# Kernel tuning notes

Hardware: AMD Instinct MI355X
Metric: run time of the kernel (lower is better)

## Reference

```python
import jax, jax.numpy as jnp
import numpy as np

N = 50000      # nodes
E = 1600000    # edges (before self loops)
G = 64         # graphs in batch
DIN = 128
HID = 64
H = 4
NEG_SLOPE = 0.2
BN_EPS = 1e-5


def setup_inputs() -> dict:
    key = jax.random.key(0)
    ks = jax.random.split(key, 32)
    p = lambda i, shape: 0.1 * jax.random.normal(ks[i], shape, dtype=jnp.float32)
    inp = {
        "x": jax.random.normal(ks[0], (N, DIN), dtype=jnp.float32),
        "edge_index": jax.random.randint(ks[1], (2, E), 0, N),
        "batch": jnp.sort(jax.random.randint(ks[2], (N,), 0, G)),
        # GAT layer 1: DIN -> HID x H heads (concat)
        "W1": p(3, (DIN, H * HID)),
        "att_src1": p(4, (H, HID)),
        "att_dst1": p(5, (H, HID)),
        "bias1": p(6, (H * HID,)),
        "bn1_g": jnp.ones((H * HID,), jnp.float32),
        "bn1_b": jnp.zeros((H * HID,), jnp.float32),
        "bn1_m": p(7, (H * HID,)),
        "bn1_v": jnp.ones((H * HID,), jnp.float32),
        # GAT layer 2: H*HID -> HID, 1 head
        "W2": p(8, (H * HID, HID)),
        "att_src2": p(9, (1, HID)),
        "att_dst2": p(10, (1, HID)),
        "bias2": p(11, (HID,)),
        "bn2_g": jnp.ones((HID,), jnp.float32),
        "bn2_b": jnp.zeros((HID,), jnp.float32),
        "bn2_m": p(12, (HID,)),
        "bn2_v": jnp.ones((HID,), jnp.float32),
        # classifier
        "Wc1": p(13, (HID, HID)),
        "bc1": p(14, (HID,)),
        "Wc2": p(15, (HID, 2)),
        "bc2": p(16, (2,)),
    }
    return inp


def _gat_layer(x, src, dst, W, a_src, a_dst, bias, heads, n):
    # x: [n, F_in]; src/dst: [E'] (self loops included)
    c = W.shape[1] // heads
    xw = (x @ W).reshape(n, heads, c)                       # [n, H, C]
    alpha_s = jnp.sum(xw * a_src, axis=-1)                  # [n, H]
    alpha_d = jnp.sum(xw * a_dst, axis=-1)                  # [n, H]
    e = alpha_s[src] + alpha_d[dst]                         # [E', H]
    e = jnp.where(e >= 0, e, NEG_SLOPE * e)                 # leaky relu
    # softmax over incoming edges of each dst node
    m = jax.ops.segment_max(e, dst, num_segments=n)         # [n, H]
    ex = jnp.exp(e - m[dst])
    denom = jax.ops.segment_sum(ex, dst, num_segments=n)    # [n, H]
    w = ex / (denom[dst] + 1e-16)                           # [E', H]
    out = jax.ops.segment_sum(xw[src] * w[:, :, None], dst, num_segments=n)
    return out.reshape(n, heads * c) + bias


def _bn_eval(x, g, b, m, v):
    return (x - m) * (g / jnp.sqrt(v + BN_EPS)) + b


def reference(x, edge_index, batch,
              W1, att_src1, att_dst1, bias1, bn1_g, bn1_b, bn1_m, bn1_v,
              W2, att_src2, att_dst2, bias2, bn2_g, bn2_b, bn2_m, bn2_v,
              Wc1, bc1, Wc2, bc2):
    n = x.shape[0]
    loops = jnp.arange(n, dtype=edge_index.dtype)
    src = jnp.concatenate([edge_index[0], loops])  # PyG GATConv adds self loops
    dst = jnp.concatenate([edge_index[1], loops])

    h = _gat_layer(x, src, dst, W1, att_src1, att_dst1, bias1, H, n)
    h = jax.nn.relu(_bn_eval(h, bn1_g, bn1_b, bn1_m, bn1_v))
    # residual skipped: dims (256) vs x (128) mismatch -> not added, as in torch code

    h2 = _gat_layer(h, src, dst, W2, att_src2, att_dst2, bias2, 1, n)
    h2 = jax.nn.relu(_bn_eval(h2, bn2_g, bn2_b, bn2_m, bn2_v))
    # residual skipped: 64 vs 256 mismatch

    # global mean pool over each graph
    sums = jax.ops.segment_sum(h2, batch, num_segments=G)
    cnt = jax.ops.segment_sum(jnp.ones((n,), h2.dtype), batch, num_segments=G)
    graph_repr = sums / jnp.maximum(cnt, 1.0)[:, None]      # [G, HID]

    hc = jax.nn.relu(graph_repr @ Wc1 + bc1)
    logits = hc @ Wc2 + bc2
    return jax.nn.log_softmax(logits, axis=1)
```

## Files before the change

### kernel.cpp

```cpp
#include <hip/hip_runtime.h>

#define NEG_SLOPE 0.2f
#define CAP1 224
#define CAP2 224
#define CAPB 5120
#define EPB  16384

typedef short bf16x8 __attribute__((ext_vector_type(8)));
typedef float f32x4  __attribute__((ext_vector_type(4)));
typedef float f32x2  __attribute__((ext_vector_type(2)));

static __device__ __forceinline__ float u16f(unsigned short u){
  union { unsigned int i; float f; } v; v.i = ((unsigned int)u) << 16; return v.f;
}
static __device__ __forceinline__ unsigned short f2u16(float f){
  union { float f; unsigned int i; } v; v.f = f;
  unsigned int r = (v.i + 0x7FFFu + ((v.i >> 16) & 1u)) >> 16;
  return (unsigned short)r;
}
static __device__ __forceinline__ unsigned char f2fp8(float f){
  int w = __builtin_amdgcn_cvt_pk_fp8_f32(f, f, 0, false);
  return (unsigned char)(w & 0xFF);
}
static __device__ __forceinline__ float fp82f(unsigned char b){
  f32x2 d = __builtin_amdgcn_cvt_pk_f32_fp8((int)b, false);
  return d[0];
}
static __device__ __forceinline__ float wsum(float v){
  #pragma unroll
  for (int o = 32; o > 0; o >>= 1) v += __shfl_xor(v, o, 64);
  return v;
}
static __device__ __forceinline__ float qsum(float v){
  #pragma unroll
  for (int o = 1; o < 16; o <<= 1) v += __shfl_xor(v, o, 64);
  return v;
}
static __device__ __forceinline__ float lrelu(float e){
  return e >= 0.f ? e : NEG_SLOPE * e;
}

__global__ __launch_bounds__(256) void k_zero(int* __restrict__ p, int nwords){
  int i = blockIdx.x * 256 + threadIdx.x;
  if (i < nwords) p[i] = 0;
}

__global__ __launch_bounds__(256) void k_cvt(const float* __restrict__ x,
                                             unsigned short* __restrict__ xb, int n4){
  int i = blockIdx.x * 256 + threadIdx.x;
  if (i >= n4) return;
  float4 f = ((const float4*)x)[i];
  ushort4 u;
  u.x = f2u16(f.x); u.y = f2u16(f.y); u.z = f2u16(f.z); u.w = f2u16(f.w);
  ((ushort4*)xb)[i] = u;
}

__global__ __launch_bounds__(256) void k_pack1(const float* __restrict__ W1,
                                               unsigned short* __restrict__ B1p){
  int idx = blockIdx.x * 256 + threadIdx.x;
  if (idx >= 4*16*64*8) return;
  int j = idx & 7, lane = (idx >> 3) & 63, nt = (idx >> 9) & 15, kc = idx >> 13;
  int k = kc*32 + (lane >> 4)*8 + j;
  int n = nt*16 + (lane & 15);
  B1p[idx] = f2u16(W1[k*256 + n]);
}

__global__ __launch_bounds__(256) void k_pack2(const float* __restrict__ W2,
                                               unsigned short* __restrict__ B2p){
  int idx = blockIdx.x * 256 + threadIdx.x;
  if (idx >= 8*4*64*8) return;
  int j = idx & 7, lane = (idx >> 3) & 63, nt = (idx >> 9) & 3, kc = idx >> 11;
  int k = kc*32 + (lane >> 4)*8 + j;
  int n = nt*16 + (lane & 15);
  B2p[idx] = f2u16(W2[k*64 + n]);
}

__global__ __launch_bounds__(256) void k_gemm1m(
    const unsigned short* __restrict__ xb, const bf16x8* __restrict__ B1p,
    const float* __restrict__ asrc, const float* __restrict__ adst,
    unsigned char* __restrict__ xw1, float* __restrict__ oas, float* __restrict__ oad,
    int N)
{
  __shared__ unsigned short xs[64][136];
  int t = threadIdx.x;
  int m0 = blockIdx.x * 64;
  #pragma unroll
  for (int i = 0; i < 4; ++i){
    int flat = t + i*256;
    int r = flat >> 4, c8 = flat & 15;
    uint4 v = make_uint4(0,0,0,0);
    if (m0 + r < N) v = *(const uint4*)(xb + (size_t)(m0 + r)*128 + c8*8);
    *(uint4*)&xs[r][c8*8] = v;
  }
  __syncthreads();
  int w = t >> 6, l = t & 63;
  int quad = l >> 4, ml = l & 15;

  f32x4 acc[16];
  #pragma unroll
  for (int i = 0; i < 16; ++i){ acc[i][0]=0.f; acc[i][1]=0.f; acc[i][2]=0.f; acc[i][3]=0.f; }

  #pragma unroll
  for (int kc = 0; kc < 4; ++kc){
    bf16x8 a = *(const bf16x8*)&xs[w*16 + ml][kc*32 + quad*8];
    #pragma unroll
    for (int nt = 0; nt < 16; ++nt){
      bf16x8 b = B1p[(kc*16 + nt)*64 + l];
      acc[nt] = __builtin_amdgcn_mfma_f32_16x16x32_bf16(a, b, acc[nt], 0, 0, 0);
    }
  }

  float as_h[4][4], ad_h[4][4];
  #pragma unroll
  for (int h = 0; h < 4; ++h)
    #pragma unroll
    for (int r = 0; r < 4; ++r){ as_h[h][r] = 0.f; ad_h[h][r] = 0.f; }
  #pragma unroll
  for (int nt = 0; nt < 16; ++nt){
    float vs = asrc[nt*16 + ml], vd = adst[nt*16 + ml];
    int h = nt >> 2;
    #pragma unroll
    for (int r = 0; r < 4; ++r){
      as_h[h][r] += acc[nt][r] * vs;
      ad_h[h][r] += acc[nt][r] * vd;
    }
  }
  #pragma unroll
  for (int h = 0; h < 4; ++h)
    #pragma unroll
    for (int r = 0; r < 4; ++r){ as_h[h][r] = qsum(as_h[h][r]); ad_h[h][r] = qsum(ad_h[h][r]); }

  int baserow = m0 + w*16 + quad*4;
  if (ml == 0){
    #pragma unroll
    for (int r = 0; r < 4; ++r){
      int node = baserow + r;
      if (node < N){
        *(float4*)(oas + (size_t)node*4) = make_float4(as_h[0][r], as_h[1][r], as_h[2][r], as_h[3][r]);
        *(float4*)(oad + (size_t)node*4) = make_float4(ad_h[0][r], ad_h[1][r], ad_h[2][r], ad_h[3][r]);
      }
    }
  }
  #pragma unroll
  for (int r = 0; r < 4; ++r){
    int node = baserow + r;
    if (node >= N) continue;
    #pragma unroll
    for (int nt = 0; nt < 16; ++nt)
      xw1[(size_t)node*256 + nt*16 + ml] = f2fp8(acc[nt][r]);
  }
}

__global__ __launch_bounds__(256) void k_gemm2m(
    const unsigned short* __restrict__ h1, const bf16x8* __restrict__ B2p,
    const float* __restrict__ asrc, const float* __restrict__ adst,
    unsigned char* __restrict__ xw2, float* __restrict__ oas, float* __restrict__ oad,
    int N)
{
  __shared__ unsigned short ys[64][264];
  int t = threadIdx.x;
  int m0 = blockIdx.x * 64;
  #pragma unroll
  for (int i = 0; i < 8; ++i){
    int flat = t + i*256;
    int r = flat >> 5, c8 = flat & 31;
    uint4 v = make_uint4(0,0,0,0);
    if (m0 + r < N) v = *(const uint4*)(h1 + (size_t)(m0 + r)*256 + c8*8);
    *(uint4*)&ys[r][c8*8] = v;
  }
  __syncthreads();
  int w = t >> 6, l = t & 63;
  int quad = l >> 4, ml = l & 15;

  f32x4 acc[4];
  #pragma unroll
  for (int i = 0; i < 4; ++i){ acc[i][0]=0.f; acc[i][1]=0.f; acc[i][2]=0.f; acc[i][3]=0.f; }

  #pragma unroll
  for (int kc = 0; kc < 8; ++kc){
    bf16x8 a = *(const bf16x8*)&ys[w*16 + ml][kc*32 + quad*8];
    #pragma unroll
    for (int nt = 0; nt < 4; ++nt){
      bf16x8 b = B2p[(kc*4 + nt)*64 + l];
      acc[nt] = __builtin_amdgcn_mfma_f32_16x16x32_bf16(a, b, acc[nt], 0, 0, 0);
    }
  }

  float as_p[4] = {0,0,0,0}, ad_p[4] = {0,0,0,0};
  #pragma unroll
  for (int nt = 0; nt < 4; ++nt){
    float vs = asrc[nt*16 + ml], vd = adst[nt*16 + ml];
    #pragma unroll
    for (int r = 0; r < 4; ++r){
      as_p[r] += acc[nt][r] * vs;
      ad_p[r] += acc[nt][r] * vd;
    }
  }
  #pragma unroll
  for (int r = 0; r < 4; ++r){ as_p[r] = qsum(as_p[r]); ad_p[r] = qsum(ad_p[r]); }

  int baserow = m0 + w*16 + quad*4;
  if (ml == 0){
    #pragma unroll
    for (int r = 0; r < 4; ++r){
      int node = baserow + r;
      if (node < N){ oas[node] = as_p[r]; oad[node] = ad_p[r]; }
    }
  }
  #pragma unroll
  for (int r = 0; r < 4; ++r){
    int node = baserow + r;
    if (node >= N) continue;
    #pragma unroll
    for (int nt = 0; nt < 4; ++nt)
      xw2[(size_t)node*64 + nt*16 + ml] = f2fp8(acc[nt][r]);
  }
}

__global__ __launch_bounds__(256) void k_hist(const int* __restrict__ ei,
                                              int* __restrict__ count, int E, int ET){
  int i = blockIdx.x * 256 + threadIdx.x;
  if (i >= ET) return;
  int d = (i < E) ? ei[E + i] : (i - E);
  atomicAdd(&count[d], 1);
}

__global__ __launch_bounds__(256) void k_scan1(const int* __restrict__ count,
                                               int* __restrict__ ro, int* __restrict__ bsum, int N){
  __shared__ int sd[256];
  int t = threadIdx.x, b = blockIdx.x, i = b*256 + t;
  int v = (i < N) ? count[i] : 0;
  sd[t] = v; __syncthreads();
  for (int o = 1; o < 256; o <<= 1){
    int x = (t >= o) ? sd[t - o] : 0;
    __syncthreads();
    sd[t] += x;
    __syncthreads();
  }
  if (i < N) ro[i] = sd[t] - v;
  if (t == 255) bsum[b] = sd[255];
}

__global__ __launch_bounds__(256) void k_scan2(int* __restrict__ bsum, int nb){
  __shared__ int sd[256];
  int t = threadIdx.x;
  int v = (t < nb) ? bsum[t] : 0;
  sd[t] = v; __syncthreads();
  for (int o = 1; o < 256; o <<= 1){
    int x = (t >= o) ? sd[t - o] : 0;
    __syncthreads();
    sd[t] += x;
    __syncthreads();
  }
  if (t < nb) bsum[t] = sd[t] - v;
}

__global__ __launch_bounds__(256) void k_scan3(int* __restrict__ ro,
                                               const int* __restrict__ bsum, int N, int ET){
  int b = blockIdx.x, t = threadIdx.x, i = b*256 + t;
  if (i < N) ro[i] += bsum[b];
  if (b == 0 && t == 0) ro[N] = ET;
}

__global__ __launch_bounds__(1024) void k_binscat(const int* __restrict__ ei,
                                                  const int* __restrict__ ro,
                                                  int* __restrict__ bincur,
                                                  int* __restrict__ binbuf,
                                                  int* __restrict__ cursor,
                                                  int* __restrict__ csr,
                                                  int E, int ET, int NB){
  __shared__ int lhist[512];
  __shared__ int lbase[512];
  __shared__ int lcur[512];
  int t = threadIdx.x;
  int base = blockIdx.x * EPB;
  for (int i = t; i < 512; i += 1024){ lhist[i] = 0; lcur[i] = 0; }
  __syncthreads();

  int myb[16], mypay[16];
  #pragma unroll
  for (int k = 0; k < 16; ++k){
    int i = base + t + k*1024;
    int b = -1, pay = 0;
    if (i < ET){
      int s, d;
      if (i < E){ s = ei[i]; d = ei[E + i]; }
      else      { s = i - E; d = i - E; }
      b = d >> 7;
      pay = ((d & 127) << 16) | s;
      atomicAdd(&lhist[b], 1);
    }
    myb[k] = b; mypay[k] = pay;
  }
  __syncthreads();

  for (int i = t; i < NB; i += 1024){
    int h = lhist[i];
    if (h > 0) lbase[i] = atomicAdd(&bincur[i * 16], h);
  }
  __syncthreads();

  #pragma unroll
  for (int k = 0; k < 16; ++k){
    int b = myb[k];
    if (b < 0) continue;
    int pos = lbase[b] + atomicAdd(&lcur[b], 1);
    if (pos < CAPB){
      binbuf[(size_t)b * CAPB + pos] = mypay[k];
    } else {
      int d = (b << 7) | (mypay[k] >> 16);
      int s = mypay[k] & 0xFFFF;
      int posr = atomicAdd(&cursor[d], 1);
      csr[ro[d + 1] - 1 - posr] = s;
    }
  }
}

__global__ __launch_bounds__(256) void k_binsort(const int* __restrict__ bincur,
                                                 const int* __restrict__ binbuf,
                                                 const int* __restrict__ ro,
                                                 int* __restrict__ csr, int N){
  __shared__ int rolocal[129];
  __shared__ int lcnt[128];
  __shared__ int stage[CAPB];
  int b = blockIdx.x, t = threadIdx.x;
  int base = b << 7;
  int wn = N - base; if (wn > 128) wn = 128;
  if (wn <= 0) return;
  for (int i = t; i <= wn; i += 256) rolocal[i] = ro[base + i];
  for (int i = t; i < wn; i += 256) lcnt[i] = 0;
  __syncthreads();
  int rostart = rolocal[0];
  int seglen = rolocal[wn] - rostart;
  int total = bincur[b * 16];
  int cnt = total < CAPB ? total : CAPB;
  bool ovf = (seglen > CAPB) || (total > CAPB);
  const int* buf = binbuf + (size_t)b * CAPB;

  if (!ovf){
    for (int i = t; i < cnt; i += 256){
      int u = buf[i];
      int s = u & 0xFFFF, ld = u >> 16;
      int r = atomicAdd(&lcnt[ld], 1);
      stage[rolocal[ld] - rostart + r] = s;
    }
    __syncthreads();
    for (int i = t; i < seglen; i += 256) csr[rostart + i] = stage[i];
  } else {
    for (int i = t; i < cnt; i += 256){
      int u = buf[i];
      int s = u & 0xFFFF, ld = u >> 16;
      int r = atomicAdd(&lcnt[ld], 1);
      csr[rolocal[ld] + r] = s;
    }
  }
}

__global__ __launch_bounds__(256) void k_edge1(
    const int* __restrict__ ro, const int* __restrict__ cs,
    const unsigned char* __restrict__ xw1,
    const float* __restrict__ pas, const float* __restrict__ pad,
    const float* __restrict__ bias1,
    const float* __restrict__ g1, const float* __restrict__ b1,
    const float* __restrict__ m1, const float* __restrict__ v1,
    unsigned short* __restrict__ h1, int N)
{
  __shared__ float wt[4][CAP1][5];
  int t = threadIdx.x, w = t >> 6, lane = t & 63;
  int n = blockIdx.x * 4 + w;
  if (n >= N) return;
  int beg = ro[n], end = ro[n + 1], deg = end - beg;
  const float4 adv = *(const float4*)(pad + (size_t)n * 4);
  const bool fits = (deg <= CAP1);

  float s0 = 0.f, s1 = 0.f, s2 = 0.f, s3 = 0.f;
  for (int j = lane; j < deg; j += 64){
    int s = cs[beg + j];
    float4 a = *(const float4*)(pas + (size_t)s * 4);
    float e0 = __expf(lrelu(a.x + adv.x));
    float e1 = __expf(lrelu(a.y + adv.y));
    float e2 = __expf(lrelu(a.z + adv.z));
    float e3 = __expf(lrelu(a.w + adv.w));
    if (fits){
      wt[w][j][0] = e0; wt[w][j][1] = e1;
      wt[w][j][2] = e2; wt[w][j][3] = e3;
      wt[w][j][4] = __int_as_float(s << 8);
    }
    s0 += e0; s1 += e1; s2 += e2; s3 += e3;
  }
  s0 = wsum(s0); s1 = wsum(s1); s2 = wsum(s2); s3 = wsum(s3);

  int head = lane >> 4;
  float invh = 1.f / ((head == 0 ? s0 : head == 1 ? s1 : head == 2 ? s2 : s3) + 1e-16f);
  float aa   = head == 0 ? adv.x : head == 1 ? adv.y : head == 2 ? adv.z : adv.w;

  float a0 = 0.f, a1 = 0.f, a2 = 0.f, a3 = 0.f;
  if (fits){
    for (int j = 0; j < deg; ++j){
      float wv = wt[w][j][head] * invh;
      int off = __float_as_int(wt[w][j][4]);
      int u = *(const int*)(xw1 + off + lane * 4);
      f32x2 lo = __builtin_amdgcn_cvt_pk_f32_fp8(u, false);
      f32x2 hi = __builtin_amdgcn_cvt_pk_f32_fp8(u, true);
      a0 += wv * lo[0]; a1 += wv * lo[1];
      a2 += wv * hi[0]; a3 += wv * hi[1];
    }
  } else {
    for (int j = 0; j < deg; ++j){
      int s = cs[beg + j];
      float wv = __expf(lrelu(pas[(size_t)s * 4 + head] + aa)) * invh;
      int u = *(const int*)(xw1 + (size_t)s * 256 + lane * 4);
      f32x2 lo = __builtin_amdgcn_cvt_pk_f32_fp8(u, false);
      f32x2 hi = __builtin_amdgcn_cvt_pk_f32_fp8(u, true);
      a0 += wv * lo[0]; a1 += wv * lo[1];
      a2 += wv * hi[0]; a3 += wv * hi[1];
    }
  }

  float accv[4] = {a0, a1, a2, a3};
  ushort4 outv;
  unsigned short* po = (unsigned short*)&outv;
  int j0 = lane * 4;
  #pragma unroll
  for (int i = 0; i < 4; ++i){
    int j = j0 + i;
    float o  = accv[i] + bias1[j];
    float sc = g1[j] * rsqrtf(v1[j] + 1e-5f);
    float res = (o - m1[j]) * sc + b1[j];
    po[i] = f2u16(fmaxf(res, 0.f));
  }
  *(ushort4*)(h1 + (size_t)n * 256 + j0) = outv;
}

__global__ __launch_bounds__(256) void k_edge2(
    const int* __restrict__ ro, const int* __restrict__ cs,
    const unsigned char* __restrict__ xw2,
    const float* __restrict__ pas, const float* __restrict__ pad,
    const float* __restrict__ bias2,
    const float* __restrict__ g2, const float* __restrict__ b2,
    const float* __restrict__ m2, const float* __restrict__ v2,
    float* __restrict__ h2, int N)
{
  __shared__ float wt[4][CAP2][2];
  int t = threadIdx.x, w = t >> 6, lane = t & 63;
  int n = blockIdx.x * 4 + w;
  if (n >= N) return;
  int beg = ro[n], end = ro[n + 1], deg = end - beg;
  float adv = pad[n];
  const bool fits = (deg <= CAP2);

  float dh = 0.f;
  for (int j = lane; j < deg; j += 64){
    int s = cs[beg + j];
    float e = __expf(lrelu(pas[s] + adv));
    if (fits){
      wt[w][j][0] = e;
      wt[w][j][1] = __int_as_float(s << 6);
    }
    dh += e;
  }
  dh = wsum(dh);
  float inv = 1.f / (dh + 1e-16f);

  float acc = 0.f;
  if (fits){
    for (int j = 0; j < deg; ++j){
      float wv = wt[w][j][0] * inv;
      int off = __float_as_int(wt[w][j][1]);
      acc += wv * fp82f(xw2[off + lane]);
    }
  } else {
    for (int j = 0; j < deg; ++j){
      int s = cs[beg + j];
      float wv = __expf(lrelu(pas[s] + adv)) * inv;
      acc += wv * fp82f(xw2[(size_t)s * 64 + lane]);
    }
  }

  float o  = acc + bias2[lane];
  float sc = g2[lane] * rsqrtf(v2[lane] + 1e-5f);
  h2[(size_t)n * 64 + lane] = fmaxf((o - m2[lane]) * sc + b2[lane], 0.f);
}

__global__ __launch_bounds__(256) void k_pool(
    const float* __restrict__ h2, const int* __restrict__ batch,
    float* __restrict__ pool, int N)
{
  int g = blockIdx.x;
  int t = threadIdx.x, c = t & 63, w = t >> 6;
  int lo = 0, hi = N;
  while (lo < hi){ int mid = (lo + hi) >> 1; if (batch[mid] < g) lo = mid + 1; else hi = mid; }
  int lo2 = lo, hi2 = N;
  while (lo2 < hi2){ int mid = (lo2 + hi2) >> 1; if (batch[mid] < g + 1) lo2 = mid + 1; else hi2 = mid; }
  float s = 0.f;
  for (int r = lo + w; r < lo2; r += 4) s += h2[(size_t)r * 64 + c];
  __shared__ float sd[4][64];
  sd[w][c] = s;
  __syncthreads();
  if (w == 0){
    float tot = sd[0][c] + sd[1][c] + sd[2][c] + sd[3][c];
    float cntf = (float)(lo2 - lo);
    pool[g * 64 + c] = tot / fmaxf(cntf, 1.f);
  }
}

__global__ __launch_bounds__(64) void k_final(
    const float* __restrict__ pool,
    const float* __restrict__ Wc1, const float* __restrict__ bc1,
    const float* __restrict__ Wc2, const float* __restrict__ bc2,
    float* __restrict__ out)
{
  int g = blockIdx.x, c = threadIdx.x;
  __shared__ float gr[64];
  gr[c] = pool[g * 64 + c];
  __syncthreads();
  float a = bc1[c];
  for (int k = 0; k < 64; ++k) a += gr[k] * Wc1[k * 64 + c];
  float hc = fmaxf(a, 0.f);
  float p0 = hc * Wc2[c * 2 + 0];
  float p1 = hc * Wc2[c * 2 + 1];
  p0 = wsum(p0); p1 = wsum(p1);
  if (c == 0){
    float l0 = p0 + bc2[0];
    float l1 = p1 + bc2[1];
    float mx = fmaxf(l0, l1);
    float lse = mx + logf(expf(l0 - mx) + expf(l1 - mx));
    out[g * 2 + 0] = l0 - lse;
    out[g * 2 + 1] = l1 - lse;
  }
}

extern "C" void kernel_launch(void* const* d_in, const int* in_sizes, int n_in,
                              void* d_out, int out_size, void* d_ws, size_t ws_size,
                              hipStream_t stream)
{
  const float* x     = (const float*)d_in[0];
  const int*   ei    = (const int*)d_in[1];
  const int*   batch = (const int*)d_in[2];
  const float* W1    = (const float*)d_in[3];
  const float* asrc1 = (const float*)d_in[4];
  const float* adst1 = (const float*)d_in[5];
  const float* bias1 = (const float*)d_in[6];
  const float* bn1g  = (const float*)d_in[7];
  const float* bn1b  = (const float*)d_in[8];
  const float* bn1m  = (const float*)d_in[9];
  const float* bn1v  = (const float*)d_in[10];
  const float* W2    = (const float*)d_in[11];
  const float* asrc2 = (const float*)d_in[12];
  const float* adst2 = (const float*)d_in[13];
  const float* bias2 = (const float*)d_in[14];
  const float* bn2g  = (const float*)d_in[15];
  const float* bn2b  = (const float*)d_in[16];
  const float* bn2m  = (const float*)d_in[17];
  const float* bn2v  = (const float*)d_in[18];
  const float* Wc1   = (const float*)d_in[19];
  const float* bc1   = (const float*)d_in[20];
  const float* Wc2   = (const float*)d_in[21];
  const float* bc2   = (const float*)d_in[22];
  float* out = (float*)d_out;

  const int N  = in_sizes[0] / 128;
  const int E  = in_sizes[1] / 2;
  const int ET = E + N;
  const int NB = (N + 127) >> 7;

  char* p = (char*)d_ws;
  auto take = [&](size_t bytes) -> void* {
    void* q = (void*)p;
    p += ((bytes + 255) & ~(size_t)255);
    return q;
  };
  int*   count  = (int*)  take((size_t)N * 4);
  int*   cursor = (int*)  take((size_t)N * 4);
  int*   bincur = (int*)  take((size_t)NB * 16 * 4);
  size_t zbytes = (size_t)(p - (char*)d_ws);
  float* pool   = (float*)take(64 * 64 * 4);
  int*   ro     = (int*)  take((size_t)(N + 1) * 4);
  int*   bsum   = (int*)  take(1024);
  float* as1    = (float*)take((size_t)N * 16);
  float* ad1    = (float*)take((size_t)N * 16);
  float* as2    = (float*)take((size_t)N * 4);
  float* ad2    = (float*)take((size_t)N * 4);
  unsigned char*  xw1 = (unsigned char*) take((size_t)N * 256);
  unsigned short* h1  = (unsigned short*)take((size_t)N * 256 * 2);
  float* h2     = (float*)take((size_t)N * 64 * 4);
  int*   csr    = (int*)  take((size_t)ET * 4);
  int*   binbuf = (int*)  take((size_t)NB * CAPB * 4);
  unsigned short* B1p = (unsigned short*)take(32768 * 2);
  unsigned short* B2p = (unsigned short*)take(16384 * 2);
  unsigned short* xb  = (unsigned short*)h2;
  unsigned char*  xw2 = xw1;
  (void)count; (void)n_in; (void)ws_size; (void)out_size;

  int zw = (int)(zbytes / 4);
  k_zero<<<dim3((zw + 255) / 256), dim3(256), 0, stream>>>((int*)d_ws, zw);
  int n4 = N * 32;
  k_cvt<<<dim3((n4 + 255) / 256), dim3(256), 0, stream>>>(x, xb, n4);
  k_pack1<<<dim3(128), dim3(256), 0, stream>>>(W1, B1p);
  k_pack2<<<dim3(64), dim3(256), 0, stream>>>(W2, B2p);
  k_hist<<<dim3((ET + 255) / 256), dim3(256), 0, stream>>>(ei, count, E, ET);
  int nb = (N + 255) / 256;
  k_scan1<<<dim3(nb), dim3(256), 0, stream>>>(count, ro, bsum, N);
  k_scan2<<<dim3(1), dim3(256), 0, stream>>>(bsum, nb);
  k_scan3<<<dim3(nb), dim3(256), 0, stream>>>(ro, bsum, N, ET);
  k_binscat<<<dim3((ET + EPB - 1) / EPB), dim3(1024), 0, stream>>>(ei, ro, bincur, binbuf,
                                                                   cursor, csr, E, ET, NB);
  k_binsort<<<dim3(NB), dim3(256), 0, stream>>>(bincur, binbuf, ro, csr, N);
  k_gemm1m<<<dim3((N + 63) / 64), dim3(256), 0, stream>>>(xb, (const bf16x8*)B1p,
                                                          asrc1, adst1, xw1, as1, ad1, N);
  k_edge1<<<dim3((N + 3) / 4), dim3(256), 0, stream>>>(ro, csr, xw1, as1, ad1,
                                                       bias1, bn1g, bn1b, bn1m, bn1v, h1, N);
  k_gemm2m<<<dim3((N + 63) / 64), dim3(256), 0, stream>>>(h1, (const bf16x8*)B2p,
                                                          asrc2, adst2, xw2, as2, ad2, N);
  k_edge2<<<dim3((N + 3) / 4), dim3(256), 0, stream>>>(ro, csr, xw2, as2, ad2,
                                                       bias2, bn2g, bn2b, bn2m, bn2v, h2, N);
  k_pool<<<dim3(64), dim3(256), 0, stream>>>(h2, batch, pool, N);
  k_final<<<dim3(64), dim3(64), 0, stream>>>(pool, Wc1, bc1, Wc2, bc2, out);
}
```

Baseline: 433.4 us.

## Derive degree counts from binned edges instead of separate histogram pass

Removes the global-atomic histogram pass over all edges. Binning now runs before the scan, and per-node counts are computed in shared memory from each bin's buffer. Edges that overflow a bin go to a separate overflow list, which gets its own count and scatter kernels. This trades one full edge read plus global atomics for two small extra kernels and a fixed overflow cap of 65536 entries. Edges beyond that cap would be silently dropped.

```diff
diff --git a/kernel.cpp b/kernel.cpp
--- a/kernel.cpp
+++ b/kernel.cpp
@@ -5,6 +5,7 @@
 #define CAP2 224
 #define CAPB 5120
 #define EPB  16384
+#define OVFCAP 65536
 
 typedef short bf16x8 __attribute__((ext_vector_type(8)));
 typedef float f32x4  __attribute__((ext_vector_type(4)));
@@ -215,14 +216,6 @@
     for (int nt = 0; nt < 4; ++nt)
       xw2[(size_t)node*64 + nt*16 + ml] = f2fp8(acc[nt][r]);
   }
-}
-
-__global__ __launch_bounds__(256) void k_hist(const int* __restrict__ ei,
-                                              int* __restrict__ count, int E, int ET){
-  int i = blockIdx.x * 256 + threadIdx.x;
-  if (i >= ET) return;
-  int d = (i < E) ? ei[E + i] : (i - E);
-  atomicAdd(&count[d], 1);
 }
 
 __global__ __launch_bounds__(256) void k_scan1(const int* __restrict__ count,
@@ -263,11 +256,10 @@
 }
 
 __global__ __launch_bounds__(1024) void k_binscat(const int* __restrict__ ei,
-                                                  const int* __restrict__ ro,
                                                   int* __restrict__ bincur,
                                                   int* __restrict__ binbuf,
-                                                  int* __restrict__ cursor,
-                                                  int* __restrict__ csr,
+                                                  int* __restrict__ ovfcnt,
+                                                  int2* __restrict__ ovfbuf,
                                                   int E, int ET, int NB){
   __shared__ int lhist[512];
   __shared__ int lbase[512];
@@ -310,9 +302,48 @@
     } else {
       int d = (b << 7) | (mypay[k] >> 16);
       int s = mypay[k] & 0xFFFF;
-      int posr = atomicAdd(&cursor[d], 1);
-      csr[ro[d + 1] - 1 - posr] = s;
-    }
+      int idx = atomicAdd(ovfcnt, 1);
+      if (idx < OVFCAP) ovfbuf[idx] = make_int2(d, s);
+    }
+  }
+}
+
+__global__ __launch_bounds__(256) void k_cnt(const int* __restrict__ bincur,
+                                             const int* __restrict__ binbuf,
+                                             int* __restrict__ count, int N){
+  __shared__ int lcnt[128];
+  int b = blockIdx.x, t = threadIdx.x;
+  int base = b << 7;
+  int wn = N - base; if (wn > 128) wn = 128;
+  if (wn <= 0) return;
+  for (int i = t; i < wn; i += 256) lcnt[i] = 0;
+  __syncthreads();
+  int total = bincur[b * 16];
+  int cnt = total < CAPB ? total : CAPB;
+  const int* buf = binbuf + (size_t)b * CAPB;
+  for (int i = t; i < cnt; i += 256) atomicAdd(&lcnt[buf[i] >> 16], 1);
+  __syncthreads();
+  for (int i = t; i < wn; i += 256) count[base + i] = lcnt[i];
+}
+
+__global__ __launch_bounds__(256) void k_cntovf(const int* __restrict__ ovfcnt,
+                                                const int2* __restrict__ ovfbuf,
+                                                int* __restrict__ count){
+  int n = ovfcnt[0]; if (n > OVFCAP) n = OVFCAP;
+  for (int i = blockIdx.x*256 + threadIdx.x; i < n; i += gridDim.x*256)
+    atomicAdd(&count[ovfbuf[i].x], 1);
+}
+
+__global__ __launch_bounds__(256) void k_ovfscat(const int* __restrict__ ovfcnt,
+                                                 const int2* __restrict__ ovfbuf,
+                                                 const int* __restrict__ ro,
+                                                 int* __restrict__ cursor,
+                                                 int* __restrict__ csr){
+  int n = ovfcnt[0]; if (n > OVFCAP) n = OVFCAP;
+  for (int i = blockIdx.x*256 + threadIdx.x; i < n; i += gridDim.x*256){
+    int d = ovfbuf[i].x, s = ovfbuf[i].y;
+    int pos = atomicAdd(&cursor[d], 1);
+    csr[ro[d + 1] - 1 - pos] = s;
   }
 }
 
@@ -570,10 +601,11 @@
     p += ((bytes + 255) & ~(size_t)255);
     return q;
   };
-  int*   count  = (int*)  take((size_t)N * 4);
   int*   cursor = (int*)  take((size_t)N * 4);
   int*   bincur = (int*)  take((size_t)NB * 16 * 4);
+  int*   ovfcnt = (int*)  take(256);
   size_t zbytes = (size_t)(p - (char*)d_ws);
+  int*   count  = (int*)  take((size_t)N * 4);
   float* pool   = (float*)take(64 * 64 * 4);
   int*   ro     = (int*)  take((size_t)(N + 1) * 4);
   int*   bsum   = (int*)  take(1024);
@@ -586,11 +618,12 @@
   float* h2     = (float*)take((size_t)N * 64 * 4);
   int*   csr    = (int*)  take((size_t)ET * 4);
   int*   binbuf = (int*)  take((size_t)NB * CAPB * 4);
+  int2*  ovfbuf = (int2*) take((size_t)OVFCAP * 8);
   unsigned short* B1p = (unsigned short*)take(32768 * 2);
   unsigned short* B2p = (unsigned short*)take(16384 * 2);
   unsigned short* xb  = (unsigned short*)h2;
   unsigned char*  xw2 = xw1;
-  (void)count; (void)n_in; (void)ws_size; (void)out_size;
+  (void)n_in; (void)ws_size; (void)out_size;
 
   int zw = (int)(zbytes / 4);
   k_zero<<<dim3((zw + 255) / 256), dim3(256), 0, stream>>>((int*)d_ws, zw);
@@ -598,14 +631,16 @@
   k_cvt<<<dim3((n4 + 255) / 256), dim3(256), 0, stream>>>(x, xb, n4);
   k_pack1<<<dim3(128), dim3(256), 0, stream>>>(W1, B1p);
   k_pack2<<<dim3(64), dim3(256), 0, stream>>>(W2, B2p);
-  k_hist<<<dim3((ET + 255) / 256), dim3(256), 0, stream>>>(ei, count, E, ET);
+  k_binscat<<<dim3((ET + EPB - 1) / EPB), dim3(1024), 0, stream>>>(ei, bincur, binbuf,
+                                                                   ovfcnt, ovfbuf, E, ET, NB);
+  k_cnt<<<dim3(NB), dim3(256), 0, stream>>>(bincur, binbuf, count, N);
+  k_cntovf<<<dim3(8), dim3(256), 0, stream>>>(ovfcnt, ovfbuf, count);
   int nb = (N + 255) / 256;
   k_scan1<<<dim3(nb), dim3(256), 0, stream>>>(count, ro, bsum, N);
   k_scan2<<<dim3(1), dim3(256), 0, stream>>>(bsum, nb);
   k_scan3<<<dim3(nb), dim3(256), 0, stream>>>(ro, bsum, N, ET);
-  k_binscat<<<dim3((ET + EPB - 1) / EPB), dim3(1024), 0, stream>>>(ei, ro, bincur, binbuf,
-                                                                   cursor, csr, E, ET, NB);
   k_binsort<<<dim3(NB), dim3(256), 0, stream>>>(bincur, binbuf, ro, csr, N);
+  k_ovfscat<<<dim3(8), dim3(256), 0, stream>>>(ovfcnt, ovfbuf, ro, cursor, csr);
   k_gemm1m<<<dim3((N + 63) / 64), dim3(256), 0, stream>>>(xb, (const bf16x8*)B1p,
                                                           asrc1, adst1, xw1, as1, ad1, N);
   k_edge1<<<dim3((N + 3) / 4), dim3(256), 0, stream>>>(ro, csr, xw1, as1, ad1,
```

Result: faster. 370.9 us (-14.4%).
